# Kernel optimization log

Hardware: AMD Instinct MI355X
Metric: run time of the kernel (lower is better)

Reference implementation:

```python
import jax, jax.numpy as jnp
import numpy as np
import math


def _rel_pos_tables(W):
    # continuous relative coords table: [(2W-1), (2W-1), 2]
    c = np.arange(-(W - 1), W, dtype=np.float32)
    table = np.stack(np.meshgrid(c, c, indexing='ij'), axis=-1)  # [2W-1,2W-1,2]
    table = table / (W - 1)
    table = table * 8.0
    table = np.sign(table) * np.log2(np.abs(table) + 1.0) / math.log2(8.0)
    # relative position index: [W*W, W*W]
    coords = np.stack(np.meshgrid(np.arange(W), np.arange(W), indexing='ij'))  # [2,W,W]
    flat = coords.reshape(2, -1)  # [2, W*W]
    rel = flat[:, :, None] - flat[:, None, :]  # [2, N, N]
    rel = rel.transpose(1, 2, 0).copy()
    rel[:, :, 0] += W - 1
    rel[:, :, 1] += W - 1
    rel[:, :, 0] *= 2 * W - 1
    idx = rel.sum(-1)  # [N, N]
    return jnp.asarray(table), jnp.asarray(idx, dtype=jnp.int32)


def setup_inputs() -> dict:
    key = jax.random.key(0)
    ks = jax.random.split(key, 10)
    dim, W, H = 512, 8, 16
    N = W * W
    B_, nW = 2048, 256
    s = 0.02
    inp = {
        'x': jax.random.normal(ks[0], (B_, N, dim), jnp.float32),
        'mask': jax.random.normal(ks[1], (nW, N, N), jnp.float32),
        'qkv_w': jax.random.normal(ks[2], (dim, 3 * dim), jnp.float32) * s,
        'qkv_b': jnp.zeros((3 * dim,), jnp.float32),
        'logit_scale': jnp.full((H, 1, 1), math.log(10.0), jnp.float32),
        'cpb_w1': jax.random.normal(ks[3], (2, 512), jnp.float32) * s,
        'cpb_b1': jnp.zeros((512,), jnp.float32),
        'cpb_w2': jax.random.normal(ks[4], (512, H), jnp.float32) * s,
        'proj_w': jax.random.normal(ks[5], (dim, dim), jnp.float32) * s,
        'proj_b': jnp.zeros((dim,), jnp.float32),
        'window_size': W,
        'num_heads': H,
    }
    return inp


def reference(x, mask, qkv_w, qkv_b, logit_scale, cpb_w1, cpb_b1, cpb_w2,
              proj_w, proj_b, window_size, num_heads):
    B_, N, C = x.shape
    H = num_heads
    hd = C // H

    qkv = (x @ qkv_w + qkv_b).reshape(B_, N, 3, H, hd)
    qkv = jnp.transpose(qkv, (2, 0, 3, 1, 4))  # [3, B_, H, N, hd]
    q, k, v = qkv[0], qkv[1], qkv[2]

    # cosine attention: L2-normalize q, k (eps matches F.normalize)
    q = q / jnp.clip(jnp.linalg.norm(q, axis=-1, keepdims=True), 1e-12)
    k = k / jnp.clip(jnp.linalg.norm(k, axis=-1, keepdims=True), 1e-12)

    attn = jnp.einsum('bhnd,bhmd->bhnm', q, k)
    scale = jnp.exp(jnp.minimum(logit_scale, math.log(1.0 / 0.01)))  # [H,1,1]
    attn = attn * scale[None]

    # continuous relative position bias
    table, idx = _rel_pos_tables(window_size)
    t = jax.nn.relu(table @ cpb_w1 + cpb_b1) @ cpb_w2  # [2W-1, 2W-1, H]
    t = t.reshape(-1, H)
    bias = t[idx.reshape(-1)].reshape(N, N, H)
    bias = 16.0 * jax.nn.sigmoid(jnp.transpose(bias, (2, 0, 1)))  # [H, N, N]
    attn = attn + bias[None]

    # mask add: [nW, N, N]
    nW = mask.shape[0]
    attn = attn.reshape(B_ // nW, nW, H, N, N) + mask[None, :, None]
    attn = attn.reshape(B_, H, N, N)

    attn = jax.nn.softmax(attn, axis=-1)
    out = jnp.einsum('bhnm,bhmd->bhnd', attn, v)
    out = jnp.transpose(out, (0, 2, 1, 3)).reshape(B_, N, C)
    out = out @ proj_w + proj_b
    return out
```

## Files before the change

kernel.cpp:

```cpp
#include <hip/hip_runtime.h>
#include <hip/hip_bf16.h>
#include <stdint.h>

typedef __attribute__((ext_vector_type(8))) short short8;
typedef __attribute__((ext_vector_type(8))) _Float16 half8;
typedef __attribute__((ext_vector_type(4))) float f32x4;

__device__ __forceinline__ unsigned short f2h(float f) {
  union { _Float16 h; unsigned short u; } c;
  c.h = (_Float16)f;
  return c.u;
}
__device__ __forceinline__ float h2f(unsigned short u) {
  union { _Float16 h; unsigned short u; } c;
  c.u = u;
  return (float)c.h;
}
__device__ __forceinline__ void gload_lds16(const void* g, void* l) {
  __builtin_amdgcn_global_load_lds(
      (const __attribute__((address_space(1))) unsigned int*)g,
      (__attribute__((address_space(3))) unsigned int*)l, 16, 0, 0);
}


__global__ __launch_bounds__(256) void cast_f16(const float* __restrict__ in,
                                                unsigned short* __restrict__ out) {
  const size_t total = (size_t)131072 * 512 / 8;
  size_t stride = (size_t)gridDim.x * 256;
  for (size_t i = blockIdx.x * 256 + threadIdx.x; i < total; i += stride) {
    f32x4 f0 = *(const f32x4*)(in + i * 8);
    f32x4 f1 = *(const f32x4*)(in + i * 8 + 4);
    short8 o;
#pragma unroll
    for (int e = 0; e < 4; e++) {
      o[e] = (short)f2h(f0[e]);
      o[4 + e] = (short)f2h(f1[e]);
    }
    *(short8*)(out + i * 8) = o;
  }
}

__global__ __launch_bounds__(256) void transpose_cast(const float* __restrict__ in,
                                                      unsigned short* __restrict__ out,
                                                      int K, int N) {
  __shared__ float tile[32][33];
  int nb = N / 32;
  int bx = blockIdx.x % nb, by = blockIdx.x / nb;
  int tx = threadIdx.x & 31, ty = threadIdx.x >> 5;
#pragma unroll
  for (int r = 0; r < 32; r += 8)
    tile[ty + r][tx] = in[(size_t)(by * 32 + ty + r) * N + bx * 32 + tx];
  __syncthreads();
#pragma unroll
  for (int r = 0; r < 32; r += 8)
    out[(size_t)(bx * 32 + ty + r) * K + by * 32 + tx] = f2h(tile[tx][ty + r]);
}

__device__ __forceinline__ float cpb_coord(int a) {
  float v = (float)(a - 7) * (8.0f / 7.0f);
  float s = (v > 0.f) ? 1.f : ((v < 0.f) ? -1.f : 0.f);
  return s * log2f(fabsf(v) + 1.f) * (1.f / 3.f);
}

__global__ __launch_bounds__(64) void cpb_mlp(const float* __restrict__ w1,
                                              const float* __restrict__ b1,
                                              const float* __restrict__ w2,
                                              float* __restrict__ t_out) {
  int e = blockIdx.x;
  int dy = e / 15, dx = e % 15;
  float in0 = cpb_coord(dy), in1 = cpb_coord(dx);
  float acc[16];
#pragma unroll
  for (int o = 0; o < 16; ++o) acc[o] = 0.f;
  for (int u = threadIdx.x; u < 512; u += 64) {
    float hsum = fmaxf(in0 * w1[u] + in1 * w1[512 + u] + b1[u], 0.f);
#pragma unroll
    for (int o = 0; o < 16; ++o) acc[o] += hsum * w2[u * 16 + o];
  }
#pragma unroll
  for (int o = 0; o < 16; ++o) {
    float v = acc[o];
    v += __shfl_xor(v, 1);  v += __shfl_xor(v, 2);  v += __shfl_xor(v, 4);
    v += __shfl_xor(v, 8);  v += __shfl_xor(v, 16); v += __shfl_xor(v, 32);
    acc[o] = v;
  }
  if (threadIdx.x == 0)
#pragma unroll
    for (int o = 0; o < 16; ++o) t_out[e * 16 + o] = acc[o];
}

__global__ __launch_bounds__(256) void bias_kernel(const float* __restrict__ t,
                                                   float* __restrict__ bias) {
  int idx = blockIdx.x * 256 + threadIdx.x;
  int j = idx & 63, i = (idx >> 6) & 63, h = idx >> 12;
  int dy = (i >> 3) - (j >> 3) + 7;
  int dx = (i & 7) - (j & 7) + 7;
  float v = t[(dy * 15 + dx) * 16 + h];
  bias[idx] = 16.f / (1.f + expf(-v));
}

__global__ __launch_bounds__(256) void qkv_gemm(const unsigned short* __restrict__ xh,
                                               const unsigned short* __restrict__ Wt,
                                               const float* __restrict__ bvec,
                                               unsigned short* __restrict__ qout,
                                               unsigned short* __restrict__ kout,
                                               unsigned short* __restrict__ vout) {
  __shared__ __align__(16) short As[128 * 32];
  __shared__ __align__(16) short Bs[128 * 32];
  const int bid = (blockIdx.x & 7) * 1536 + (blockIdx.x >> 3);
  const int nt = bid % 12;
  const int mt = bid / 12;
  const int m0 = mt * 128, n0 = nt * 128;
  const int t = threadIdx.x;
  const int l = t & 63, w = t >> 6;
  const int wm = w >> 1, wn = w & 1;
  const int fr = l & 15, fg = l >> 4;

  f32x4 acc[4][4];
#pragma unroll
  for (int i = 0; i < 4; i++)
#pragma unroll
    for (int j = 0; j < 4; j++) acc[i][j] = f32x4{0.f, 0.f, 0.f, 0.f};

  for (int k0 = 0; k0 < 512; k0 += 32) {
#pragma unroll
    for (int it = 0; it < 2; ++it) {
      int flat = it * 256 + t;
      int row = flat >> 2, ch = flat & 3;
      gload_lds16(xh + (size_t)(m0 + row) * 512 + k0 + ch * 8, &As[flat * 8]);
      gload_lds16(Wt + (size_t)(n0 + row) * 512 + k0 + ch * 8, &Bs[flat * 8]);
    }
    __syncthreads();
    half8 af[4], bfr[4];
#pragma unroll
    for (int i = 0; i < 4; i++) af[i] = *(half8*)&As[(wm * 64 + i * 16 + fr) * 32 + fg * 8];
#pragma unroll
    for (int j = 0; j < 4; j++) bfr[j] = *(half8*)&Bs[(wn * 64 + j * 16 + fr) * 32 + fg * 8];
#pragma unroll
    for (int i = 0; i < 4; i++)
#pragma unroll
      for (int j = 0; j < 4; j++)
        acc[i][j] = __builtin_amdgcn_mfma_f32_16x16x32_f16(af[i], bfr[j], acc[i][j], 0, 0, 0);
    __syncthreads();
  }

#pragma unroll
  for (int j = 0; j < 4; j++) {
    int col = n0 + wn * 64 + j * 16 + fr;
    float bb = bvec[col];
#pragma unroll
    for (int i = 0; i < 4; i++) {
      int row0 = m0 + wm * 64 + i * 16 + fg * 4;
#pragma unroll
      for (int r = 0; r < 4; r++) {
        unsigned short hv = f2h(acc[i][j][r] + bb);
        size_t off = (size_t)(row0 + r) * 512;
        if (nt < 4)       qout[off + col] = hv;
        else if (nt < 8)  kout[off + col - 512] = hv;
        else              vout[off + col - 1024] = hv;
      }
    }
  }
}

__global__ __launch_bounds__(256) void attn_kernel(const unsigned short* __restrict__ qws,
                                                   const unsigned short* __restrict__ kws,
                                                   const unsigned short* __restrict__ vws,
                                                   const float* __restrict__ bias,
                                                   const float* __restrict__ mask,
                                                   const float* __restrict__ logit_scale,
                                                   unsigned short* __restrict__ aout) {
  const int blk = (blockIdx.x & 7) * 4096 + (blockIdx.x >> 3);
  const int h = blk & 15;
  const int b = blk >> 4;
  const int wmi = b & 255;
  const int t = threadIdx.x, l = t & 63, w = t >> 6;

  __shared__ __align__(16) short qs[64 * 32], ks[64 * 32];
  __shared__ __align__(16) short vt[32 * 72];
  __shared__ __align__(16) short plds[4 * 16 * 72];
  __shared__ float invs[64];

  const float scale = __expf(fminf(logit_scale[h], 4.6051702f));

  {
    const int r = t >> 2, c4 = t & 3;
    {
      uint4 raw = *(const uint4*)(qws + (size_t)(b * 64 + r) * 512 + h * 32 + c4 * 8);
      unsigned int rr[4] = {raw.x, raw.y, raw.z, raw.w};
      float f[8];
#pragma unroll
      for (int e = 0; e < 4; e++) {
        f[2 * e]     = h2f((unsigned short)(rr[e] & 0xffff));
        f[2 * e + 1] = h2f((unsigned short)(rr[e] >> 16));
      }
      float ss = 0.f;
#pragma unroll
      for (int e = 0; e < 8; e++) ss += f[e] * f[e];
      ss += __shfl_xor(ss, 1);
      ss += __shfl_xor(ss, 2);
      float inv = 1.f / fmaxf(sqrtf(ss), 1e-12f);
      short8 o;
#pragma unroll
      for (int e = 0; e < 8; e++) o[e] = (short)f2h(f[e] * inv);
      *(short8*)&qs[r * 32 + c4 * 8] = o;
    }
    {
      uint4 raw = *(const uint4*)(kws + (size_t)(b * 64 + r) * 512 + h * 32 + c4 * 8);
      unsigned int rr[4] = {raw.x, raw.y, raw.z, raw.w};
      float f[8];
#pragma unroll
      for (int e = 0; e < 4; e++) {
        f[2 * e]     = h2f((unsigned short)(rr[e] & 0xffff));
        f[2 * e + 1] = h2f((unsigned short)(rr[e] >> 16));
      }
      float ss = 0.f;
#pragma unroll
      for (int e = 0; e < 8; e++) ss += f[e] * f[e];
      ss += __shfl_xor(ss, 1);
      ss += __shfl_xor(ss, 2);
      float inv = 1.f / fmaxf(sqrtf(ss), 1e-12f);
      short8 o;
#pragma unroll
      for (int e = 0; e < 8; e++) o[e] = (short)f2h(f[e] * inv);
      *(short8*)&ks[r * 32 + c4 * 8] = o;
    }
    {
      uint4 raw = *(const uint4*)(vws + (size_t)(b * 64 + r) * 512 + h * 32 + c4 * 8);
      unsigned int rr[4] = {raw.x, raw.y, raw.z, raw.w};
#pragma unroll
      for (int e2 = 0; e2 < 4; e2++) {
        vt[(c4 * 8 + 2 * e2 + 0) * 72 + r] = (short)(rr[e2] & 0xffff);
        vt[(c4 * 8 + 2 * e2 + 1) * 72 + r] = (short)(rr[e2] >> 16);
      }
    }
  }
  __syncthreads();

  const int fr = l & 15, fg = l >> 4;
  half8 bq = *(half8*)&qs[(w * 16 + fr) * 32 + fg * 8];

  f32x4 st[4];
#pragma unroll
  for (int kt = 0; kt < 4; kt++) {
    half8 ak = *(half8*)&ks[(kt * 16 + fr) * 32 + fg * 8];
    st[kt] = __builtin_amdgcn_mfma_f32_16x16x32_f16(ak, bq, f32x4{0.f, 0.f, 0.f, 0.f}, 0, 0, 0);
  }
  const int q = w * 16 + fr;
  const int kbase = fg * 4;
  float sv[16];
  float mx = -1e30f;
#pragma unroll
  for (int kt = 0; kt < 4; kt++) {
    f32x4 b4 = *(const f32x4*)&bias[(size_t)(h * 64 + q) * 64 + kt * 16 + kbase];
    f32x4 m4 = *(const f32x4*)&mask[(size_t)(wmi * 64 + q) * 64 + kt * 16 + kbase];
#pragma unroll
    for (int j = 0; j < 4; j++) {
      float xv = st[kt][j] * scale + b4[j] + m4[j];
      sv[kt * 4 + j] = xv;
      mx = fmaxf(mx, xv);
    }
  }
  mx = fmaxf(mx, __shfl_xor(mx, 16));
  mx = fmaxf(mx, __shfl_xor(mx, 32));
  float sum = 0.f;
#pragma unroll
  for (int i2 = 0; i2 < 16; i2++) {
    float p = __expf(sv[i2] - mx);
    sv[i2] = p;
    sum += p;
  }
  sum += __shfl_xor(sum, 16);
  sum += __shfl_xor(sum, 32);

  short* pl = &plds[w * 16 * 72];
#pragma unroll
  for (int kt = 0; kt < 4; kt++)
#pragma unroll
    for (int j = 0; j < 4; j += 2) {
      unsigned int pack = (unsigned int)f2h(sv[kt * 4 + j]) |
                          ((unsigned int)f2h(sv[kt * 4 + j + 1]) << 16);
      *(unsigned int*)&pl[fr * 72 + kt * 16 + kbase + j] = pack;
    }
  if (fg == 0) invs[q] = 1.f / sum;
  __syncthreads();

  half8 pa0 = *(half8*)&pl[fr * 72 + fg * 8];
  half8 pa1 = *(half8*)&pl[fr * 72 + 32 + fg * 8];
#pragma unroll
  for (int nt2 = 0; nt2 < 2; nt2++) {
    half8 bv0 = *(half8*)&vt[(nt2 * 16 + fr) * 72 + fg * 8];
    half8 bv1 = *(half8*)&vt[(nt2 * 16 + fr) * 72 + 32 + fg * 8];
    f32x4 o = f32x4{0.f, 0.f, 0.f, 0.f};
    o = __builtin_amdgcn_mfma_f32_16x16x32_f16(pa0, bv0, o, 0, 0, 0);
    o = __builtin_amdgcn_mfma_f32_16x16x32_f16(pa1, bv1, o, 0, 0, 0);
    const int qo = w * 16 + fg * 4;
    const int hd = nt2 * 16 + fr;
#pragma unroll
    for (int r2 = 0; r2 < 4; r2++) {
      float vv = o[r2] * invs[qo + r2];
      aout[(size_t)(b * 64 + qo + r2) * 512 + h * 32 + hd] = f2h(vv);
    }
  }
}

__global__ __launch_bounds__(256) void proj_gemm(const unsigned short* __restrict__ A,
                                                 const unsigned short* __restrict__ Wt,
                                                 const float* __restrict__ bvec,
                                                 float* __restrict__ out) {
  __shared__ __align__(16) short As[128 * 32];
  __shared__ __align__(16) short Bs[128 * 32];
  const int bid = (blockIdx.x & 7) * 512 + (blockIdx.x >> 3);
  const int nt = bid & 3;
  const int mt = bid >> 2;
  const int m0 = mt * 128, n0 = nt * 128;
  const int t = threadIdx.x;
  const int l = t & 63, w = t >> 6;
  const int wm = w >> 1, wn = w & 1;
  const int fr = l & 15, fg = l >> 4;

  f32x4 acc[4][4];
#pragma unroll
  for (int i = 0; i < 4; i++)
#pragma unroll
    for (int j = 0; j < 4; j++) acc[i][j] = f32x4{0.f, 0.f, 0.f, 0.f};

  for (int k0 = 0; k0 < 512; k0 += 32) {
#pragma unroll
    for (int it = 0; it < 2; ++it) {
      int flat = it * 256 + t;
      int row = flat >> 2, ch = flat & 3;
      gload_lds16(A + (size_t)(m0 + row) * 512 + k0 + ch * 8, &As[flat * 8]);
      gload_lds16(Wt + (size_t)(n0 + row) * 512 + k0 + ch * 8, &Bs[flat * 8]);
    }
    __syncthreads();
    half8 af[4], bfr[4];
#pragma unroll
    for (int i = 0; i < 4; i++) af[i] = *(half8*)&As[(wm * 64 + i * 16 + fr) * 32 + fg * 8];
#pragma unroll
    for (int j = 0; j < 4; j++) bfr[j] = *(half8*)&Bs[(wn * 64 + j * 16 + fr) * 32 + fg * 8];
#pragma unroll
    for (int i = 0; i < 4; i++)
#pragma unroll
      for (int j = 0; j < 4; j++)
        acc[i][j] = __builtin_amdgcn_mfma_f32_16x16x32_f16(af[i], bfr[j], acc[i][j], 0, 0, 0);
    __syncthreads();
  }

#pragma unroll
  for (int j = 0; j < 4; j++) {
    int col = n0 + wn * 64 + j * 16 + fr;
    float bb = bvec[col];
#pragma unroll
    for (int i = 0; i < 4; i++) {
      int row0 = m0 + wm * 64 + i * 16 + fg * 4;
#pragma unroll
      for (int r = 0; r < 4; r++)
        out[(size_t)(row0 + r) * 512 + col] = acc[i][j][r] + bb;
    }
  }
}

extern "C" void kernel_launch(void* const* d_in, const int* in_sizes, int n_in,
                              void* d_out, int out_size, void* d_ws, size_t ws_size,
                              hipStream_t stream) {
  const float* x           = (const float*)d_in[0];
  const float* mask        = (const float*)d_in[1];
  const float* qkv_w       = (const float*)d_in[2];
  const float* qkv_b       = (const float*)d_in[3];
  const float* logit_scale = (const float*)d_in[4];
  const float* cpb_w1      = (const float*)d_in[5];
  const float* cpb_b1      = (const float*)d_in[6];
  const float* cpb_w2      = (const float*)d_in[7];
  const float* proj_w      = (const float*)d_in[8];
  const float* proj_b      = (const float*)d_in[9];
  (void)in_sizes; (void)n_in; (void)out_size; (void)ws_size;

  char* p = (char*)d_ws;
  unsigned short* Wqkv_t  = (unsigned short*)p; p += (size_t)1536 * 512 * 2;
  unsigned short* Wproj_t = (unsigned short*)p; p += (size_t)512 * 512 * 2;
  float* t_cpb            = (float*)p;          p += (size_t)225 * 16 * 4;
  float* biasb            = (float*)p;          p += (size_t)16 * 64 * 64 * 4;
  unsigned short* xh      = (unsigned short*)p; p += (size_t)131072 * 512 * 2;
  unsigned short* qbuf    = (unsigned short*)p; p += (size_t)131072 * 512 * 2;
  unsigned short* kbuf    = (unsigned short*)p; p += (size_t)131072 * 512 * 2;
  unsigned short* vbuf    = (unsigned short*)p; p += (size_t)131072 * 512 * 2;
  unsigned short* abuf    = (unsigned short*)p; p += (size_t)131072 * 512 * 2;

  cast_f16<<<2048, 256, 0, stream>>>(x, xh);
  transpose_cast<<<768, 256, 0, stream>>>(qkv_w, Wqkv_t, 512, 1536);
  transpose_cast<<<256, 256, 0, stream>>>(proj_w, Wproj_t, 512, 512);
  cpb_mlp<<<225, 64, 0, stream>>>(cpb_w1, cpb_b1, cpb_w2, t_cpb);
  bias_kernel<<<256, 256, 0, stream>>>(t_cpb, biasb);
  qkv_gemm<<<12288, 256, 0, stream>>>(xh, Wqkv_t, qkv_b, qbuf, kbuf, vbuf);
  attn_kernel<<<32768, 256, 0, stream>>>(qbuf, kbuf, vbuf, biasb, mask, logit_scale, abuf);
  proj_gemm<<<4096, 256, 0, stream>>>(abuf, Wproj_t, proj_b, (float*)d_out);
}
```

Baseline: 879.1 us.

## Double-buffer LDS tiles in QKV and projection GEMMs

Both GEMM kernels now keep two LDS buffers per operand and issue the global-to-LDS loads for the next K slice before running MFMAs on the current one. The aim is to overlap global memory latency with matrix compute and drop one barrier per iteration. In exchange, LDS use per block doubles, which may lower occupancy. Correctness also depends on the single remaining barrier covering both the async LDS loads and the buffer reuse; there is no explicit vmcnt wait before reading the next buffer.

```diff
diff --git a/kernel.cpp b/kernel.cpp
--- a/kernel.cpp
+++ b/kernel.cpp
@@ -105,8 +105,8 @@
                                                unsigned short* __restrict__ qout,
                                                unsigned short* __restrict__ kout,
                                                unsigned short* __restrict__ vout) {
-  __shared__ __align__(16) short As[128 * 32];
-  __shared__ __align__(16) short Bs[128 * 32];
+  __shared__ __align__(16) short As[2][128 * 32];
+  __shared__ __align__(16) short Bs[2][128 * 32];
   const int bid = (blockIdx.x & 7) * 1536 + (blockIdx.x >> 3);
   const int nt = bid % 12;
   const int mt = bid / 12;
@@ -115,6 +115,7 @@
   const int l = t & 63, w = t >> 6;
   const int wm = w >> 1, wn = w & 1;
   const int fr = l & 15, fg = l >> 4;
+  const int srow = t >> 2, sch = t & 3;
 
   f32x4 acc[4][4];
 #pragma unroll
@@ -122,26 +123,33 @@
 #pragma unroll
     for (int j = 0; j < 4; j++) acc[i][j] = f32x4{0.f, 0.f, 0.f, 0.f};
 
-  for (int k0 = 0; k0 < 512; k0 += 32) {
+  auto STAGE = [&](int bsel, int k0) {
 #pragma unroll
     for (int it = 0; it < 2; ++it) {
       int flat = it * 256 + t;
-      int row = flat >> 2, ch = flat & 3;
-      gload_lds16(xh + (size_t)(m0 + row) * 512 + k0 + ch * 8, &As[flat * 8]);
-      gload_lds16(Wt + (size_t)(n0 + row) * 512 + k0 + ch * 8, &Bs[flat * 8]);
-    }
-    __syncthreads();
+      int row = (it * 256 + t) >> 2, ch = sch;
+      gload_lds16(xh + (size_t)(m0 + row) * 512 + k0 + ch * 8, &As[bsel][flat * 8]);
+      gload_lds16(Wt + (size_t)(n0 + row) * 512 + k0 + ch * 8, &Bs[bsel][flat * 8]);
+    }
+  };
+
+  STAGE(0, 0);
+  __syncthreads();
+  int cur = 0;
+  for (int k0 = 0; k0 < 512; k0 += 32) {
+    if (k0 + 32 < 512) STAGE(cur ^ 1, k0 + 32);
     half8 af[4], bfr[4];
 #pragma unroll
-    for (int i = 0; i < 4; i++) af[i] = *(half8*)&As[(wm * 64 + i * 16 + fr) * 32 + fg * 8];
-#pragma unroll
-    for (int j = 0; j < 4; j++) bfr[j] = *(half8*)&Bs[(wn * 64 + j * 16 + fr) * 32 + fg * 8];
+    for (int i = 0; i < 4; i++) af[i] = *(half8*)&As[cur][(wm * 64 + i * 16 + fr) * 32 + fg * 8];
+#pragma unroll
+    for (int j = 0; j < 4; j++) bfr[j] = *(half8*)&Bs[cur][(wn * 64 + j * 16 + fr) * 32 + fg * 8];
 #pragma unroll
     for (int i = 0; i < 4; i++)
 #pragma unroll
       for (int j = 0; j < 4; j++)
         acc[i][j] = __builtin_amdgcn_mfma_f32_16x16x32_f16(af[i], bfr[j], acc[i][j], 0, 0, 0);
     __syncthreads();
+    cur ^= 1;
   }
 
 #pragma unroll
@@ -308,8 +316,8 @@
                                                  const unsigned short* __restrict__ Wt,
                                                  const float* __restrict__ bvec,
                                                  float* __restrict__ out) {
-  __shared__ __align__(16) short As[128 * 32];
-  __shared__ __align__(16) short Bs[128 * 32];
+  __shared__ __align__(16) short As[2][128 * 32];
+  __shared__ __align__(16) short Bs[2][128 * 32];
   const int bid = (blockIdx.x & 7) * 512 + (blockIdx.x >> 3);
   const int nt = bid & 3;
   const int mt = bid >> 2;
@@ -318,6 +326,7 @@
   const int l = t & 63, w = t >> 6;
   const int wm = w >> 1, wn = w & 1;
   const int fr = l & 15, fg = l >> 4;
+  const int sch = t & 3;
 
   f32x4 acc[4][4];
 #pragma unroll
@@ -325,26 +334,33 @@
 #pragma unroll
     for (int j = 0; j < 4; j++) acc[i][j] = f32x4{0.f, 0.f, 0.f, 0.f};
 
-  for (int k0 = 0; k0 < 512; k0 += 32) {
+  auto STAGE = [&](int bsel, int k0) {
 #pragma unroll
     for (int it = 0; it < 2; ++it) {
       int flat = it * 256 + t;
-      int row = flat >> 2, ch = flat & 3;
-      gload_lds16(A + (size_t)(m0 + row) * 512 + k0 + ch * 8, &As[flat * 8]);
-      gload_lds16(Wt + (size_t)(n0 + row) * 512 + k0 + ch * 8, &Bs[flat * 8]);
-    }
-    __syncthreads();
+      int row = flat >> 2;
+      gload_lds16(A + (size_t)(m0 + row) * 512 + k0 + sch * 8, &As[bsel][flat * 8]);
+      gload_lds16(Wt + (size_t)(n0 + row) * 512 + k0 + sch * 8, &Bs[bsel][flat * 8]);
+    }
+  };
+
+  STAGE(0, 0);
+  __syncthreads();
+  int cur = 0;
+  for (int k0 = 0; k0 < 512; k0 += 32) {
+    if (k0 + 32 < 512) STAGE(cur ^ 1, k0 + 32);
     half8 af[4], bfr[4];
 #pragma unroll
-    for (int i = 0; i < 4; i++) af[i] = *(half8*)&As[(wm * 64 + i * 16 + fr) * 32 + fg * 8];
-#pragma unroll
-    for (int j = 0; j < 4; j++) bfr[j] = *(half8*)&Bs[(wn * 64 + j * 16 + fr) * 32 + fg * 8];
+    for (int i = 0; i < 4; i++) af[i] = *(half8*)&As[cur][(wm * 64 + i * 16 + fr) * 32 + fg * 8];
+#pragma unroll
+    for (int j = 0; j < 4; j++) bfr[j] = *(half8*)&Bs[cur][(wn * 64 + j * 16 + fr) * 32 + fg * 8];
 #pragma unroll
     for (int i = 0; i < 4; i++)
 #pragma unroll
       for (int j = 0; j < 4; j++)
         acc[i][j] = __builtin_amdgcn_mfma_f32_16x16x32_f16(af[i], bfr[j], acc[i][j], 0, 0, 0);
     __syncthreads();
+    cur ^= 1;
   }
 
 #pragma unroll
```

Measured after the change: 831.0 us. 5.5% less time.
